# Optimization experiments

Measured on AMD Instinct MI355X. Metric: run time of the kernel, lower is better.

## Reference

```python
import jax, jax.numpy as jnp
import numpy as np


def sparsemax(z, axis=0):
    # Standard sparsemax projection onto the simplex (Martins & Astudillo 2016).
    n = z.shape[axis]
    # shift by max for numerical stability (invariant for sparsemax)
    z = z - jnp.max(z, axis=axis, keepdims=True)
    z_sorted = -jnp.sort(-z, axis=axis)  # descending sort along axis
    z_cumsum = jnp.cumsum(z_sorted, axis=axis)
    k_shape = [1] * z.ndim
    k_shape[axis] = n
    k = jnp.arange(1, n + 1, dtype=z.dtype).reshape(k_shape)
    support = (1.0 + k * z_sorted) > z_cumsum  # in-support mask
    k_sup = jnp.sum(support, axis=axis, keepdims=True)  # support size (int)
    # cumsum value at index k_sup-1 along axis
    cs_k = jnp.take_along_axis(z_cumsum, k_sup - 1, axis=axis)
    tau = (cs_k - 1.0) / k_sup.astype(z.dtype)
    return jnp.maximum(z - tau, 0.0)


def setup_inputs() -> dict:
    key = jax.random.key(0)
    k_x, k_a = jax.random.split(key)
    x = jax.random.normal(k_x, (4096, 8192), dtype=jnp.float32)
    a = jnp.asarray(1.0, dtype=jnp.float32)  # nn.Parameter initialized to 1.0
    return {"x": x, "a": a}


def reference(x, a):
    z = -jnp.exp(a) * x
    return sparsemax(z, axis=0)
```

## Files before the change

### kernel.cpp

```cpp
#include <hip/hip_runtime.h>
#include <math.h>


constexpr int ROWS = 4096;
constexpr int COLS = 8192;
constexpr int TPB  = 1024;
constexpr int CPB  = 16;
constexpr int RPT  = 16;
constexpr int WPB  = TPB / 64;
constexpr int CAP  = 64;
constexpr int MSTR = 20;
constexpr int FSTR = 36;

__global__ __launch_bounds__(TPB, 4)
void sparsemax_cols(const float* __restrict__ x, const float* __restrict__ a,
                    float* __restrict__ out)
{
    __shared__ float red[WPB * MSTR];
    __shared__ float m_col[CPB];
    __shared__ float cand[CPB][CAP];
    __shared__ int   cnt[CPB];
    __shared__ int   overflow;
    __shared__ float tauLDS[CPB];
    __shared__ float fred[WPB * FSTR];
    __shared__ float ffin[32];

    const int tid  = threadIdx.x;
    const int cq   = tid & 3;
    const int rg   = tid >> 2;
    const int lane = tid & 63;
    const int wave = tid >> 6;

    if (tid < CPB) cnt[tid] = 0;
    if (tid == 0)  overflow = 0;

    const long col = (long)blockIdx.x * CPB + cq * 4;
    const float s  = -expf(a[0]);

    float z[RPT][4];
    #pragma unroll
    for (int k = 0; k < RPT; ++k) {
        const long row = rg + k * 256;
        const float4 v = *reinterpret_cast<const float4*>(x + row * COLS + col);
        z[k][0] = s * v.x; z[k][1] = s * v.y;
        z[k][2] = s * v.z; z[k][3] = s * v.w;
    }
    #pragma unroll
    for (int k = 0; k < RPT; ++k) {
        asm volatile("" : "+v"(z[k][0]), "+v"(z[k][1]),
                          "+v"(z[k][2]), "+v"(z[k][3]));
    }

    float pm[4] = {z[0][0], z[0][1], z[0][2], z[0][3]};
    #pragma unroll
    for (int k = 1; k < RPT; ++k) {
        #pragma unroll
        for (int c = 0; c < 4; ++c) pm[c] = fmaxf(pm[c], z[k][c]);
    }
    #pragma unroll
    for (int m = 4; m < 64; m <<= 1) {
        #pragma unroll
        for (int c = 0; c < 4; ++c) pm[c] = fmaxf(pm[c], __shfl_xor(pm[c], m, 64));
    }
    if (lane < 4) {
        #pragma unroll
        for (int c = 0; c < 4; ++c) red[wave * MSTR + lane * 4 + c] = pm[c];
    }
    __syncthreads();
    if (tid < CPB) {
        float m = red[tid];
        #pragma unroll
        for (int w = 1; w < WPB; ++w) m = fmaxf(m, red[w * MSTR + tid]);
        m_col[tid] = m;
    }
    __syncthreads();

    float thr[4];
    #pragma unroll
    for (int c = 0; c < 4; ++c) thr[c] = m_col[cq * 4 + c] - 1.0f;
    #pragma unroll
    for (int k = 0; k < RPT; ++k) {
        #pragma unroll
        for (int c = 0; c < 4; ++c) {
            const float v = z[k][c];
            if (v > thr[c]) {
                const int ci  = cq * 4 + c;
                const int idx = atomicAdd(&cnt[ci], 1);
                if (idx < CAP) cand[ci][idx] = v;
                else           overflow = 1;
            }
        }
    }
    __syncthreads();

    float tau[4];
    if (!overflow) {
        const int K = min(cnt[wave], CAP);
        const float v = (lane < K) ? cand[wave][lane] : -3.3e38f;
        float t = -3.0e38f, prev = 0.f;
        for (int it = 0; it < CAP + 2; ++it) {
            const bool act = v > t;
            float ssum = act ? v : 0.f;
            float scnt = act ? 1.f : 0.f;
            #pragma unroll
            for (int m = 1; m < 64; m <<= 1) {
                ssum += __shfl_xor(ssum, m, 64);
                scnt += __shfl_xor(scnt, m, 64);
            }
            t = (ssum - 1.0f) / scnt;
            if (scnt == prev) break;
            prev = scnt;
        }
        if (lane == 0) tauLDS[wave] = t;
        __syncthreads();
        #pragma unroll
        for (int c = 0; c < 4; ++c) tau[c] = tauLDS[cq * 4 + c];
    } else {
        float t4[4]    = {-1e30f, -1e30f, -1e30f, -1e30f};
        float prevc[4] = {-1.f, -1.f, -1.f, -1.f};
        for (int it = 0; it < 80; ++it) {
            float ps[4] = {0.f, 0.f, 0.f, 0.f};
            float pc[4] = {0.f, 0.f, 0.f, 0.f};
            #pragma unroll
            for (int k = 0; k < RPT; ++k) {
                #pragma unroll
                for (int c = 0; c < 4; ++c) {
                    if (z[k][c] > t4[c]) { ps[c] += z[k][c]; pc[c] += 1.f; }
                }
            }
            #pragma unroll
            for (int m = 4; m < 64; m <<= 1) {
                #pragma unroll
                for (int c = 0; c < 4; ++c) {
                    ps[c] += __shfl_xor(ps[c], m, 64);
                    pc[c] += __shfl_xor(pc[c], m, 64);
                }
            }
            if (lane < 4) {
                float* dst = fred + wave * FSTR + lane * 8;
                *reinterpret_cast<float4*>(dst)     = make_float4(ps[0], ps[1], ps[2], ps[3]);
                *reinterpret_cast<float4*>(dst + 4) = make_float4(pc[0], pc[1], pc[2], pc[3]);
            }
            __syncthreads();
            if (tid < 32) {
                float t = 0.f;
                #pragma unroll
                for (int w = 0; w < WPB; ++w) t += fred[w * FSTR + tid];
                ffin[tid] = t;
            }
            __syncthreads();
            const float4 ts = *reinterpret_cast<const float4*>(ffin + cq * 8);
            const float4 tc = *reinterpret_cast<const float4*>(ffin + cq * 8 + 4);
            t4[0] = (ts.x - 1.0f) / tc.x;
            t4[1] = (ts.y - 1.0f) / tc.y;
            t4[2] = (ts.z - 1.0f) / tc.z;
            t4[3] = (ts.w - 1.0f) / tc.w;
            int done = (tc.x == prevc[0]) & (tc.y == prevc[1]) &
                       (tc.z == prevc[2]) & (tc.w == prevc[3]);
            prevc[0] = tc.x; prevc[1] = tc.y; prevc[2] = tc.z; prevc[3] = tc.w;
            if (__syncthreads_and(done)) break;
        }
        #pragma unroll
        for (int c = 0; c < 4; ++c) tau[c] = t4[c];
    }

    #pragma unroll
    for (int k = 0; k < RPT; ++k) {
        const long row = rg + k * 256;
        float4 o;
        o.x = fmaxf(z[k][0] - tau[0], 0.f);
        o.y = fmaxf(z[k][1] - tau[1], 0.f);
        o.z = fmaxf(z[k][2] - tau[2], 0.f);
        o.w = fmaxf(z[k][3] - tau[3], 0.f);
        *reinterpret_cast<float4*>(out + row * COLS + col) = o;
    }
}

extern "C" void kernel_launch(void* const* d_in, const int* in_sizes, int n_in,
                              void* d_out, int out_size, void* d_ws, size_t ws_size,
                              hipStream_t stream) {
    const float* x = (const float*)d_in[0];
    const float* a = (const float*)d_in[1];
    float* out = (float*)d_out;
    hipLaunchKernelGGL(sparsemax_cols, dim3(COLS / CPB), dim3(TPB), 0, stream,
                       x, a, out);
}
```

Before: 285.3 us.

## Split sparsemax into gather, per-column solve and elementwise epilogue kernels

Replaces the single fused per-column kernel with three kernels. The first computes per-row-block column maxima and appends candidates above that local max minus one to global per-column buffers via atomics. The second solves tau per column with one wave each, falling back to a strided full-column scan if a column overflows. The third is a grid-stride elementwise pass that re-reads x. This exposes far more parallelism than the column-sliced launch, at the cost of reading x twice, extra launches, and a slow fallback whenever a column collects more than 64 candidates.

New measurement: 264.5 us. -7.3%, faster.

```diff
diff --git a/kernel.cpp b/kernel.cpp
--- a/kernel.cpp
+++ b/kernel.cpp
@@ -4,105 +4,101 @@
 
 constexpr int ROWS = 4096;
 constexpr int COLS = 8192;
-constexpr int TPB  = 1024;
-constexpr int CPB  = 16;
-constexpr int RPT  = 16;
-constexpr int WPB  = TPB / 64;
 constexpr int CAP  = 64;
-constexpr int MSTR = 20;
-constexpr int FSTR = 36;
 
-__global__ __launch_bounds__(TPB, 4)
-void sparsemax_cols(const float* __restrict__ x, const float* __restrict__ a,
-                    float* __restrict__ out)
+constexpr int CB = 32;
+constexpr int RB = 512;
+constexpr int T1 = 512;
+constexpr int KK = RB / 64;
+
+__global__ __launch_bounds__(T1, 4)
+void k1_gather(const float* __restrict__ x, const float* __restrict__ a,
+               int* __restrict__ cnt, float* __restrict__ cand)
 {
-    __shared__ float red[WPB * MSTR];
-    __shared__ float m_col[CPB];
-    __shared__ float cand[CPB][CAP];
-    __shared__ int   cnt[CPB];
-    __shared__ int   overflow;
-    __shared__ float tauLDS[CPB];
-    __shared__ float fred[WPB * FSTR];
-    __shared__ float ffin[32];
+    __shared__ float wmax[8][33];
+    __shared__ float mcol[CB];
 
     const int tid  = threadIdx.x;
-    const int cq   = tid & 3;
-    const int rg   = tid >> 2;
+    const int cq   = tid & 7;
+    const int rg   = tid >> 3;
     const int lane = tid & 63;
     const int wave = tid >> 6;
 
-    if (tid < CPB) cnt[tid] = 0;
-    if (tid == 0)  overflow = 0;
+    const int  colb = blockIdx.x * CB;
+    const long col  = colb + cq * 4;
+    const int  row0 = blockIdx.y * RB;
+    const float s   = -expf(a[0]);
 
-    const long col = (long)blockIdx.x * CPB + cq * 4;
-    const float s  = -expf(a[0]);
-
-    float z[RPT][4];
-    #pragma unroll
-    for (int k = 0; k < RPT; ++k) {
-        const long row = rg + k * 256;
+    float z[KK][4];
+#pragma unroll
+    for (int k = 0; k < KK; ++k) {
+        const long row = row0 + rg + k * 64;
         const float4 v = *reinterpret_cast<const float4*>(x + row * COLS + col);
         z[k][0] = s * v.x; z[k][1] = s * v.y;
         z[k][2] = s * v.z; z[k][3] = s * v.w;
     }
-    #pragma unroll
-    for (int k = 0; k < RPT; ++k) {
+#pragma unroll
+    for (int k = 0; k < KK; ++k)
         asm volatile("" : "+v"(z[k][0]), "+v"(z[k][1]),
                           "+v"(z[k][2]), "+v"(z[k][3]));
-    }
 
     float pm[4] = {z[0][0], z[0][1], z[0][2], z[0][3]};
-    #pragma unroll
-    for (int k = 1; k < RPT; ++k) {
-        #pragma unroll
+#pragma unroll
+    for (int k = 1; k < KK; ++k)
+#pragma unroll
         for (int c = 0; c < 4; ++c) pm[c] = fmaxf(pm[c], z[k][c]);
-    }
-    #pragma unroll
-    for (int m = 4; m < 64; m <<= 1) {
-        #pragma unroll
+#pragma unroll
+    for (int m = 8; m < 64; m <<= 1)
+#pragma unroll
         for (int c = 0; c < 4; ++c) pm[c] = fmaxf(pm[c], __shfl_xor(pm[c], m, 64));
-    }
-    if (lane < 4) {
-        #pragma unroll
-        for (int c = 0; c < 4; ++c) red[wave * MSTR + lane * 4 + c] = pm[c];
+    if (lane < 8) {
+#pragma unroll
+        for (int c = 0; c < 4; ++c) wmax[wave][lane * 4 + c] = pm[c];
     }
     __syncthreads();
-    if (tid < CPB) {
-        float m = red[tid];
-        #pragma unroll
-        for (int w = 1; w < WPB; ++w) m = fmaxf(m, red[w * MSTR + tid]);
-        m_col[tid] = m;
+    if (tid < CB) {
+        float m = wmax[0][tid];
+#pragma unroll
+        for (int w = 1; w < 8; ++w) m = fmaxf(m, wmax[w][tid]);
+        mcol[tid] = m;
     }
     __syncthreads();
 
     float thr[4];
-    #pragma unroll
-    for (int c = 0; c < 4; ++c) thr[c] = m_col[cq * 4 + c] - 1.0f;
-    #pragma unroll
-    for (int k = 0; k < RPT; ++k) {
-        #pragma unroll
+#pragma unroll
+    for (int c = 0; c < 4; ++c) thr[c] = mcol[cq * 4 + c] - 1.0f;
+#pragma unroll
+    for (int k = 0; k < KK; ++k)
+#pragma unroll
         for (int c = 0; c < 4; ++c) {
             const float v = z[k][c];
             if (v > thr[c]) {
-                const int ci  = cq * 4 + c;
+                const int ci  = colb + cq * 4 + c;
                 const int idx = atomicAdd(&cnt[ci], 1);
-                if (idx < CAP) cand[ci][idx] = v;
-                else           overflow = 1;
+                if (idx < CAP) cand[(long)ci * CAP + idx] = v;
             }
         }
-    }
-    __syncthreads();
+}
 
-    float tau[4];
-    if (!overflow) {
-        const int K = min(cnt[wave], CAP);
-        const float v = (lane < K) ? cand[wave][lane] : -3.3e38f;
-        float t = -3.0e38f, prev = 0.f;
+__global__ __launch_bounds__(256)
+void k2_solve(const int* __restrict__ cnt, const float* __restrict__ cand,
+              const float* __restrict__ x, const float* __restrict__ a,
+              float* __restrict__ tau)
+{
+    const int lane = threadIdx.x & 63;
+    const int wave = threadIdx.x >> 6;
+    const int col  = blockIdx.x * 4 + wave;
+    const int K    = cnt[col];
+
+    float t = -3.0e38f;
+    if (K <= CAP) {
+        const float v = (lane < K) ? cand[(long)col * CAP + lane] : -3.3e38f;
+        float prev = 0.f;
         for (int it = 0; it < CAP + 2; ++it) {
             const bool act = v > t;
             float ssum = act ? v : 0.f;
             float scnt = act ? 1.f : 0.f;
-            #pragma unroll
+#pragma unroll
             for (int m = 1; m < 64; m <<= 1) {
                 ssum += __shfl_xor(ssum, m, 64);
                 scnt += __shfl_xor(scnt, m, 64);
@@ -111,68 +107,47 @@
             if (scnt == prev) break;
             prev = scnt;
         }
-        if (lane == 0) tauLDS[wave] = t;
-        __syncthreads();
-        #pragma unroll
-        for (int c = 0; c < 4; ++c) tau[c] = tauLDS[cq * 4 + c];
     } else {
-        float t4[4]    = {-1e30f, -1e30f, -1e30f, -1e30f};
-        float prevc[4] = {-1.f, -1.f, -1.f, -1.f};
-        for (int it = 0; it < 80; ++it) {
-            float ps[4] = {0.f, 0.f, 0.f, 0.f};
-            float pc[4] = {0.f, 0.f, 0.f, 0.f};
-            #pragma unroll
-            for (int k = 0; k < RPT; ++k) {
-                #pragma unroll
-                for (int c = 0; c < 4; ++c) {
-                    if (z[k][c] > t4[c]) { ps[c] += z[k][c]; pc[c] += 1.f; }
-                }
+        const float s = -expf(a[0]);
+        float prev = 0.f;
+        for (int it = 0; it < 256; ++it) {
+            float ssum = 0.f, scnt = 0.f;
+            for (int i = 0; i < ROWS / 64; ++i) {
+                const float zz = s * x[(long)(lane + i * 64) * COLS + col];
+                if (zz > t) { ssum += zz; scnt += 1.f; }
             }
-            #pragma unroll
-            for (int m = 4; m < 64; m <<= 1) {
-                #pragma unroll
-                for (int c = 0; c < 4; ++c) {
-                    ps[c] += __shfl_xor(ps[c], m, 64);
-                    pc[c] += __shfl_xor(pc[c], m, 64);
-                }
+#pragma unroll
+            for (int m = 1; m < 64; m <<= 1) {
+                ssum += __shfl_xor(ssum, m, 64);
+                scnt += __shfl_xor(scnt, m, 64);
             }
-            if (lane < 4) {
-                float* dst = fred + wave * FSTR + lane * 8;
-                *reinterpret_cast<float4*>(dst)     = make_float4(ps[0], ps[1], ps[2], ps[3]);
-                *reinterpret_cast<float4*>(dst + 4) = make_float4(pc[0], pc[1], pc[2], pc[3]);
-            }
-            __syncthreads();
-            if (tid < 32) {
-                float t = 0.f;
-                #pragma unroll
-                for (int w = 0; w < WPB; ++w) t += fred[w * FSTR + tid];
-                ffin[tid] = t;
-            }
-            __syncthreads();
-            const float4 ts = *reinterpret_cast<const float4*>(ffin + cq * 8);
-            const float4 tc = *reinterpret_cast<const float4*>(ffin + cq * 8 + 4);
-            t4[0] = (ts.x - 1.0f) / tc.x;
-            t4[1] = (ts.y - 1.0f) / tc.y;
-            t4[2] = (ts.z - 1.0f) / tc.z;
-            t4[3] = (ts.w - 1.0f) / tc.w;
-            int done = (tc.x == prevc[0]) & (tc.y == prevc[1]) &
-                       (tc.z == prevc[2]) & (tc.w == prevc[3]);
-            prevc[0] = tc.x; prevc[1] = tc.y; prevc[2] = tc.z; prevc[3] = tc.w;
-            if (__syncthreads_and(done)) break;
+            t = (ssum - 1.0f) / scnt;
+            if (scnt == prev) break;
+            prev = scnt;
         }
-        #pragma unroll
-        for (int c = 0; c < 4; ++c) tau[c] = t4[c];
     }
+    if (lane == 0) tau[col] = t;
+}
 
-    #pragma unroll
-    for (int k = 0; k < RPT; ++k) {
-        const long row = rg + k * 256;
+__global__ __launch_bounds__(256, 8)
+void k3_epilogue(const float* __restrict__ x, const float* __restrict__ a,
+                 const float* __restrict__ tau, float* __restrict__ out)
+{
+    const float s = -expf(a[0]);
+    const float4* x4 = reinterpret_cast<const float4*>(x);
+    const float4* t4 = reinterpret_cast<const float4*>(tau);
+    float4*       o4 = reinterpret_cast<float4*>(out);
+    const int N4 = ROWS * (COLS / 4);
+    const int stride = gridDim.x * blockDim.x;
+    for (int i = blockIdx.x * blockDim.x + threadIdx.x; i < N4; i += stride) {
+        const float4 v  = x4[i];
+        const float4 tt = t4[i & (COLS / 4 - 1)];
         float4 o;
-        o.x = fmaxf(z[k][0] - tau[0], 0.f);
-        o.y = fmaxf(z[k][1] - tau[1], 0.f);
-        o.z = fmaxf(z[k][2] - tau[2], 0.f);
-        o.w = fmaxf(z[k][3] - tau[3], 0.f);
-        *reinterpret_cast<float4*>(out + row * COLS + col) = o;
+        o.x = fmaxf(fmaf(s, v.x, -tt.x), 0.f);
+        o.y = fmaxf(fmaf(s, v.y, -tt.y), 0.f);
+        o.z = fmaxf(fmaf(s, v.z, -tt.z), 0.f);
+        o.w = fmaxf(fmaf(s, v.w, -tt.w), 0.f);
+        o4[i] = o;
     }
 }
 
@@ -182,6 +157,17 @@
     const float* x = (const float*)d_in[0];
     const float* a = (const float*)d_in[1];
     float* out = (float*)d_out;
-    hipLaunchKernelGGL(sparsemax_cols, dim3(COLS / CPB), dim3(TPB), 0, stream,
-                       x, a, out);
+
+    char*  ws   = (char*)d_ws;
+    int*   cnt  = (int*)ws;
+    float* tau  = (float*)(ws + 32 * 1024);
+    float* cand = (float*)(ws + 64 * 1024);
+
+    hipMemsetAsync(cnt, 0, COLS * sizeof(int), stream);
+    hipLaunchKernelGGL(k1_gather, dim3(COLS / CB, ROWS / RB), dim3(T1), 0, stream,
+                       x, a, cnt, cand);
+    hipLaunchKernelGGL(k2_solve, dim3(COLS / 4), dim3(256), 0, stream,
+                       cnt, cand, x, a, tau);
+    hipLaunchKernelGGL(k3_epilogue, dim3(2048), dim3(256), 0, stream,
+                       x, a, tau, out);
 }
```
